# Performance work log

Measured on AMD Instinct MI355X. Metric: run time of the kernel, lower is better.

Reference implementation:

```python
import jax, jax.numpy as jnp
import numpy as np

HIDDEN = 1024
HEADS = 16
HEAD_DIM = HIDDEN // HEADS

def setup_inputs() -> dict:
    key = jax.random.key(0)
    k1, k2, k3 = jax.random.split(key, 3)
    scale = 1.0 / np.sqrt(HIDDEN)
    return {
        "x": jax.random.normal(k1, (2, 2048, HIDDEN), dtype=jnp.float32),
        "w_qkv": jax.random.normal(k2, (HIDDEN, 3 * HIDDEN), dtype=jnp.float32) * scale,
        "b_qkv": jnp.zeros((3 * HIDDEN,), dtype=jnp.float32),
        "w_out": jax.random.normal(k3, (HIDDEN, HIDDEN), dtype=jnp.float32) * scale,
        "b_out": jnp.zeros((HIDDEN,), dtype=jnp.float32),
    }

def reference(x, w_qkv, b_qkv, w_out, b_out):
    B, S, H = x.shape
    qkv = x @ w_qkv + b_qkv                              # (B,S,3H)
    qkv = qkv.reshape(B, S, 3, HEADS, HEAD_DIM)
    qkv = jnp.transpose(qkv, (2, 0, 3, 1, 4))            # (3,B,nh,S,hd)
    q, k, v = qkv[0], qkv[1], qkv[2]
    scores = jnp.einsum("bhqd,bhkd->bhqk", q, k) / np.sqrt(HEAD_DIM)
    causal = jnp.triu(jnp.ones((S, S), dtype=bool), k=1)  # True above diagonal
    scores = jnp.where(causal, -jnp.inf, scores)
    attn = jax.nn.softmax(scores, axis=-1)               # dropout: eval mode (identity)
    out = jnp.einsum("bhqk,bhkd->bhqd", attn, v)
    out = jnp.transpose(out, (0, 2, 1, 3)).reshape(B, S, H)
    return out @ w_out + b_out
```

## Files before the change

kernel.cpp:

```cpp
#include <hip/hip_runtime.h>
#include <hip/hip_bf16.h>

typedef short short8 __attribute__((ext_vector_type(8)));
typedef float f32x4 __attribute__((ext_vector_type(4)));

__device__ __forceinline__ unsigned short f2bf(float f) {
    unsigned int u = __builtin_bit_cast(unsigned int, f);
    u += 0x7fff + ((u >> 16) & 1);
    return (unsigned short)(u >> 16);
}

__global__ __launch_bounds__(256) void cast_f32_bf16(
    const float* __restrict__ in, unsigned short* __restrict__ out, int n)
{
    int i = (blockIdx.x * 256 + threadIdx.x) * 4;
    if (i >= n) return;
    float4 v = *(const float4*)(in + i);
    ushort4 o;
    o.x = f2bf(v.x); o.y = f2bf(v.y); o.z = f2bf(v.z); o.w = f2bf(v.w);
    *(ushort4*)(out + i) = o;
}

__global__ __launch_bounds__(256) void transpose_cast(
    const float* __restrict__ w, unsigned short* __restrict__ wt, int K, int N)
{
    __shared__ unsigned short tile[64 * 65];
    int k0 = blockIdx.y * 64, n0 = blockIdx.x * 64;
    for (int i = threadIdx.x; i < 64 * 64; i += 256) {
        int r = i >> 6, c = i & 63;
        tile[r * 65 + c] = f2bf(w[(size_t)(k0 + r) * N + n0 + c]);
    }
    __syncthreads();
    for (int i = threadIdx.x; i < 64 * 64; i += 256) {
        int r = i >> 6, c = i & 63;
        wt[(size_t)(n0 + r) * K + k0 + c] = tile[c * 65 + r];
    }
}

#define LDSS 40

template<bool OUT_BF16, bool QKV>
__global__ __launch_bounds__(256) void gemm_bt(
    const unsigned short* __restrict__ A,
    const unsigned short* __restrict__ Bt,
    const float* __restrict__ bias,
    void* __restrict__ C,
    unsigned short* __restrict__ vTp,
    int M, int N, int K)
{
    __shared__ __align__(16) unsigned short As[128 * LDSS];
    __shared__ __align__(16) unsigned short Bs[128 * LDSS];
    const int tid = threadIdx.x;
    const int lane = tid & 63;
    const int wave = tid >> 6;
    const int wr = wave >> 1, wc = wave & 1;
    const int m0 = blockIdx.x * 128, n0 = blockIdx.y * 128;
    const int fr = lane & 15, fq = lane >> 4;

    f32x4 acc[4][4] = {};

    const int sr = tid >> 2;
    const int sc = (tid & 3) * 8;

    for (int k0 = 0; k0 < K; k0 += 32) {
        uint4 a0 = *(const uint4*)(A  + (size_t)(m0 + sr)      * K + k0 + sc);
        uint4 a1 = *(const uint4*)(A  + (size_t)(m0 + sr + 64) * K + k0 + sc);
        uint4 b0 = *(const uint4*)(Bt + (size_t)(n0 + sr)      * K + k0 + sc);
        uint4 b1 = *(const uint4*)(Bt + (size_t)(n0 + sr + 64) * K + k0 + sc);
        __syncthreads();
        *(uint4*)(As + sr * LDSS + sc)        = a0;
        *(uint4*)(As + (sr + 64) * LDSS + sc) = a1;
        *(uint4*)(Bs + sr * LDSS + sc)        = b0;
        *(uint4*)(Bs + (sr + 64) * LDSS + sc) = b1;
        __syncthreads();

        short8 af[4], bfr[4];
#pragma unroll
        for (int i = 0; i < 4; i++)
            af[i] = *(const short8*)(As + (wr * 64 + i * 16 + fr) * LDSS + fq * 8);
#pragma unroll
        for (int j = 0; j < 4; j++)
            bfr[j] = *(const short8*)(Bs + (wc * 64 + j * 16 + fr) * LDSS + fq * 8);
#pragma unroll
        for (int i = 0; i < 4; i++)
#pragma unroll
            for (int j = 0; j < 4; j++)
                acc[i][j] = __builtin_amdgcn_mfma_f32_16x16x32_bf16(af[i], bfr[j], acc[i][j], 0, 0, 0);
    }

#pragma unroll
    for (int i = 0; i < 4; i++)
#pragma unroll
        for (int j = 0; j < 4; j++) {
            int col = n0 + wc * 64 + j * 16 + fr;
            float bv = bias[col];
            if (QKV && col >= 2048) {
                int hh = (col - 2048) >> 6, d = col & 63;
#pragma unroll
                for (int r = 0; r < 4; r++) {
                    int row = m0 + wr * 64 + i * 16 + fq * 4 + r;
                    int bb = row >> 11, s = row & 2047;
                    vTp[((size_t)(bb * 16 + hh) * 64 + d) * 2048 + s] = f2bf(acc[i][j][r] + bv);
                }
            } else {
#pragma unroll
                for (int r = 0; r < 4; r++) {
                    int row = m0 + wr * 64 + i * 16 + fq * 4 + r;
                    float v = acc[i][j][r] + bv;
                    if (OUT_BF16)
                        ((unsigned short*)C)[(size_t)row * N + col] = f2bf(v);
                    else
                        ((float*)C)[(size_t)row * N + col] = v;
                }
            }
        }
}


template<int RG0>
__device__ __forceinline__ void attn_step(
    const unsigned short* __restrict__ Ksb,
    const unsigned short* __restrict__ Vsb,
    unsigned short* __restrict__ Psw,
    const short8 (&qf)[2][2], const short8 ones,
    f32x4 (&o_acc)[2][4], f32x4 (&l_acc)[2],
    int j0, int fr, int fq,
    const int (&qrow0)[2], const bool (&diag)[2])
{
    f32x4 s[2][4];
#pragma unroll
    for (int rg = RG0; rg < 2; rg++)
#pragma unroll
        for (int t = 0; t < 4; t++)
            s[rg][t] = (f32x4){0.f, 0.f, 0.f, 0.f};

#pragma unroll
    for (int t = 0; t < 4; t++)
#pragma unroll
        for (int ks = 0; ks < 2; ks++) {
            short8 kf = *(const short8*)(Ksb + (t * 16 + fr) * 72 + ks * 32 + fq * 8);
#pragma unroll
            for (int rg = RG0; rg < 2; rg++)
                s[rg][t] = __builtin_amdgcn_mfma_f32_16x16x32_bf16(qf[rg][ks], kf, s[rg][t], 0, 0, 0);
        }

#pragma unroll
    for (int rg = RG0; rg < 2; rg++) {
#pragma unroll
        for (int t = 0; t < 4; t++)
#pragma unroll
            for (int r = 0; r < 4; r++) {
                float p = __expf(s[rg][t][r] * 0.125f - 8.0f);
                if (diag[rg]) {
                    int kcol = j0 + t * 16 + fr;
                    if (kcol > qrow0[rg] + fq * 4 + r) p = 0.f;
                }
                Psw[rg * (16 * 72) + (fq * 4 + r) * 72 + t * 16 + fr] = f2bf(p);
            }
    }

#pragma unroll
    for (int ks = 0; ks < 2; ks++) {
        short8 pf[2];
#pragma unroll
        for (int rg = RG0; rg < 2; rg++)
            pf[rg] = *(const short8*)(Psw + rg * (16 * 72) + fr * 72 + ks * 32 + fq * 8);
#pragma unroll
        for (int t = 0; t < 4; t++) {
            short8 vf = *(const short8*)(Vsb + (t * 16 + fr) * 72 + ks * 32 + fq * 8);
#pragma unroll
            for (int rg = RG0; rg < 2; rg++)
                o_acc[rg][t] = __builtin_amdgcn_mfma_f32_16x16x32_bf16(pf[rg], vf, o_acc[rg][t], 0, 0, 0);
        }
#pragma unroll
        for (int rg = RG0; rg < 2; rg++)
            l_acc[rg] = __builtin_amdgcn_mfma_f32_16x16x32_bf16(pf[rg], ones, l_acc[rg], 0, 0, 0);
    }
}

__global__ __launch_bounds__(256) void flash_attn(
    const unsigned short* __restrict__ qkv,
    const unsigned short* __restrict__ vT,
    unsigned short* __restrict__ out)
{
    const int bx = blockIdx.x, h = blockIdx.y, b = blockIdx.z;
    const int qtA = bx, qtB = 31 - bx;
    const int tid = threadIdx.x, wave = tid >> 6, lane = tid & 63;
    const int fr = lane & 15, fq = lane >> 4;
    const size_t RS = 3072;

    const unsigned short* Qb = qkv + (size_t)b * 2048 * RS + h * 64;
    const unsigned short* Kb = Qb + 1024;
    const unsigned short* Vt = vT + (size_t)(b * 16 + h) * 64 * 2048;

    __shared__ __align__(16) unsigned short Ks[2][64 * 72];
    __shared__ __align__(16) unsigned short Vs[2][64 * 72];
    __shared__ __align__(16) unsigned short Ps[4][2 * 16 * 72];

    short8 qf[2][2];
    int qrow0[2];
#pragma unroll
    for (int rg = 0; rg < 2; rg++) {
        int qt = rg ? qtB : qtA;
        qrow0[rg] = qt * 64 + wave * 16;
        const unsigned short* qrow = Qb + (size_t)(qrow0[rg] + fr) * RS;
        qf[rg][0] = *(const short8*)(qrow + fq * 8);
        qf[rg][1] = *(const short8*)(qrow + 32 + fq * 8);
    }
    short8 ones;
#pragma unroll
    for (int e = 0; e < 8; e++) ones[e] = (short)0x3F80;

    f32x4 o_acc[2][4] = {};
    f32x4 l_acc[2] = {};

    const int sr = tid >> 3;
    const int sc = (tid & 7) * 8;
    const int njt = qtB + 1;

    uint4 rk0, rk1, rv0, rv1;
    rk0 = *(const uint4*)(Kb + (size_t)sr * RS + sc);
    rk1 = *(const uint4*)(Kb + (size_t)(sr + 32) * RS + sc);
    rv0 = *(const uint4*)(Vt + (size_t)sr * 2048 + sc);
    rv1 = *(const uint4*)(Vt + (size_t)(sr + 32) * 2048 + sc);
    *(uint4*)(Ks[0] + sr * 72 + sc)        = rk0;
    *(uint4*)(Ks[0] + (sr + 32) * 72 + sc) = rk1;
    *(uint4*)(Vs[0] + sr * 72 + sc)        = rv0;
    *(uint4*)(Vs[0] + (sr + 32) * 72 + sc) = rv1;

    for (int jt = 0; jt < njt; jt++) {
        const int cur = jt & 1;
        const int j0 = jt * 64;
        const bool more = (jt + 1 < njt);
        if (more) {
            const int jn = j0 + 64;
            rk0 = *(const uint4*)(Kb + (size_t)(jn + sr) * RS + sc);
            rk1 = *(const uint4*)(Kb + (size_t)(jn + sr + 32) * RS + sc);
            rv0 = *(const uint4*)(Vt + (size_t)sr * 2048 + jn + sc);
            rv1 = *(const uint4*)(Vt + (size_t)(sr + 32) * 2048 + jn + sc);
        }
        __syncthreads();
        bool diag[2] = { jt == qtA, jt == qtB };
        if (jt <= qtA)
            attn_step<0>(Ks[cur], Vs[cur], Ps[wave], qf, ones, o_acc, l_acc, j0, fr, fq, qrow0, diag);
        else
            attn_step<1>(Ks[cur], Vs[cur], Ps[wave], qf, ones, o_acc, l_acc, j0, fr, fq, qrow0, diag);
        if (more) {
            const int nb = cur ^ 1;
            *(uint4*)(Ks[nb] + sr * 72 + sc)        = rk0;
            *(uint4*)(Ks[nb] + (sr + 32) * 72 + sc) = rk1;
            *(uint4*)(Vs[nb] + sr * 72 + sc)        = rv0;
            *(uint4*)(Vs[nb] + (sr + 32) * 72 + sc) = rv1;
        }
    }

#pragma unroll
    for (int rg = 0; rg < 2; rg++)
#pragma unroll
        for (int t = 0; t < 4; t++)
#pragma unroll
            for (int r = 0; r < 4; r++) {
                int row = qrow0[rg] + fq * 4 + r;
                out[(size_t)(b * 2048 + row) * 1024 + h * 64 + t * 16 + fr] =
                    f2bf(o_acc[rg][t][r] / l_acc[rg][r]);
            }
}

extern "C" void kernel_launch(void* const* d_in, const int* in_sizes, int n_in,
                              void* d_out, int out_size, void* d_ws, size_t ws_size,
                              hipStream_t stream) {
    const float* x      = (const float*)d_in[0];
    const float* w_qkv  = (const float*)d_in[1];
    const float* b_qkv  = (const float*)d_in[2];
    const float* w_out  = (const float*)d_in[3];
    const float* b_out  = (const float*)d_in[4];
    float* out = (float*)d_out;

    char* ws = (char*)d_ws;
    unsigned short* x_b    = (unsigned short*)(ws);
    unsigned short* wqkv_t = (unsigned short*)(ws + 8u  * 1024 * 1024);
    unsigned short* wout_t = (unsigned short*)(ws + 14u * 1024 * 1024);
    unsigned short* qkv    = (unsigned short*)(ws + 16u * 1024 * 1024);
    unsigned short* attn   = (unsigned short*)(ws + 40u * 1024 * 1024);
    unsigned short* vT     = (unsigned short*)(ws + 48u * 1024 * 1024);

    cast_f32_bf16<<<4096, 256, 0, stream>>>(x, x_b, 2 * 2048 * 1024);
    transpose_cast<<<dim3(48, 16), 256, 0, stream>>>(w_qkv, wqkv_t, 1024, 3072);
    transpose_cast<<<dim3(16, 16), 256, 0, stream>>>(w_out, wout_t, 1024, 1024);
    gemm_bt<true, true ><<<dim3(32, 24), 256, 0, stream>>>(x_b,  wqkv_t, b_qkv, qkv, vT, 4096, 3072, 1024);
    flash_attn<<<dim3(16, 16, 2), 256, 0, stream>>>(qkv, vT, attn);
    gemm_bt<false, false><<<dim3(32, 8),  256, 0, stream>>>(attn, wout_t, b_out, out, nullptr, 4096, 1024, 1024);
}
```

Baseline: 208.0 us.

## Use direct global-to-LDS async loads in GEMM and attention, pack P stores

```diff
diff --git a/kernel.cpp b/kernel.cpp
--- a/kernel.cpp
+++ b/kernel.cpp
@@ -3,11 +3,20 @@
 
 typedef short short8 __attribute__((ext_vector_type(8)));
 typedef float f32x4 __attribute__((ext_vector_type(4)));
+
+typedef const __attribute__((address_space(1))) unsigned int* gas_ptr;
+typedef __attribute__((address_space(3))) unsigned int* las_ptr;
+#define ASYNC16(g, l) __builtin_amdgcn_global_load_lds((gas_ptr)(g), (las_ptr)(l), 16, 0, 0)
 
 __device__ __forceinline__ unsigned short f2bf(float f) {
     unsigned int u = __builtin_bit_cast(unsigned int, f);
     u += 0x7fff + ((u >> 16) & 1);
     return (unsigned short)(u >> 16);
+}
+
+__device__ __forceinline__ unsigned int pkbf_trunc(float lo, float hi) {
+    return __builtin_amdgcn_perm(__builtin_bit_cast(unsigned int, hi),
+                                 __builtin_bit_cast(unsigned int, lo), 0x07060302u);
 }
 
 __global__ __launch_bounds__(256) void cast_f32_bf16(
@@ -37,10 +46,9 @@
     }
 }
 
-#define LDSS 40
 
 template<bool OUT_BF16, bool QKV>
-__global__ __launch_bounds__(256) void gemm_bt(
+__global__ __launch_bounds__(256, 3) void gemm_bt(
     const unsigned short* __restrict__ A,
     const unsigned short* __restrict__ Bt,
     const float* __restrict__ bias,
@@ -48,8 +56,8 @@
     unsigned short* __restrict__ vTp,
     int M, int N, int K)
 {
-    __shared__ __align__(16) unsigned short As[128 * LDSS];
-    __shared__ __align__(16) unsigned short Bs[128 * LDSS];
+    __shared__ __align__(16) unsigned short As[128 * 32];
+    __shared__ __align__(16) unsigned short Bs[128 * 32];
     const int tid = threadIdx.x;
     const int lane = tid & 63;
     const int wave = tid >> 6;
@@ -59,28 +67,30 @@
 
     f32x4 acc[4][4] = {};
 
-    const int sr = tid >> 2;
-    const int sc = (tid & 3) * 8;
+    const int grow = lane >> 2;
+    const int gcol = (lane & 3) * 8;
+    const unsigned short* Ag = A  + (size_t)(m0 + wave * 32 + grow) * K + gcol;
+    const unsigned short* Bg = Bt + (size_t)(n0 + wave * 32 + grow) * K + gcol;
+    unsigned short* AsW0 = As + (wave * 32) * 32;
+    unsigned short* AsW1 = As + (wave * 32 + 16) * 32;
+    unsigned short* BsW0 = Bs + (wave * 32) * 32;
+    unsigned short* BsW1 = Bs + (wave * 32 + 16) * 32;
 
     for (int k0 = 0; k0 < K; k0 += 32) {
-        uint4 a0 = *(const uint4*)(A  + (size_t)(m0 + sr)      * K + k0 + sc);
-        uint4 a1 = *(const uint4*)(A  + (size_t)(m0 + sr + 64) * K + k0 + sc);
-        uint4 b0 = *(const uint4*)(Bt + (size_t)(n0 + sr)      * K + k0 + sc);
-        uint4 b1 = *(const uint4*)(Bt + (size_t)(n0 + sr + 64) * K + k0 + sc);
         __syncthreads();
-        *(uint4*)(As + sr * LDSS + sc)        = a0;
-        *(uint4*)(As + (sr + 64) * LDSS + sc) = a1;
-        *(uint4*)(Bs + sr * LDSS + sc)        = b0;
-        *(uint4*)(Bs + (sr + 64) * LDSS + sc) = b1;
+        ASYNC16(Ag + k0,          AsW0);
+        ASYNC16(Ag + 16 * K + k0, AsW1);
+        ASYNC16(Bg + k0,          BsW0);
+        ASYNC16(Bg + 16 * K + k0, BsW1);
         __syncthreads();
 
         short8 af[4], bfr[4];
 #pragma unroll
         for (int i = 0; i < 4; i++)
-            af[i] = *(const short8*)(As + (wr * 64 + i * 16 + fr) * LDSS + fq * 8);
+            af[i] = *(const short8*)(As + (wr * 64 + i * 16 + fr) * 32 + fq * 8);
 #pragma unroll
         for (int j = 0; j < 4; j++)
-            bfr[j] = *(const short8*)(Bs + (wc * 64 + j * 16 + fr) * LDSS + fq * 8);
+            bfr[j] = *(const short8*)(Bs + (wc * 64 + j * 16 + fr) * 32 + fq * 8);
 #pragma unroll
         for (int i = 0; i < 4; i++)
 #pragma unroll
@@ -119,8 +129,8 @@
 
 template<int RG0>
 __device__ __forceinline__ void attn_step(
-    const unsigned short* __restrict__ Ksb,
-    const unsigned short* __restrict__ Vsb,
+    const unsigned short* __restrict__ Ks0, const unsigned short* __restrict__ Ks1,
+    const unsigned short* __restrict__ Vs0, const unsigned short* __restrict__ Vs1,
     unsigned short* __restrict__ Psw,
     const short8 (&qf)[2][2], const short8 ones,
     f32x4 (&o_acc)[2][4], f32x4 (&l_acc)[2],
@@ -135,39 +145,48 @@
             s[rg][t] = (f32x4){0.f, 0.f, 0.f, 0.f};
 
 #pragma unroll
-    for (int t = 0; t < 4; t++)
-#pragma unroll
-        for (int ks = 0; ks < 2; ks++) {
-            short8 kf = *(const short8*)(Ksb + (t * 16 + fr) * 72 + ks * 32 + fq * 8);
-#pragma unroll
-            for (int rg = RG0; rg < 2; rg++)
-                s[rg][t] = __builtin_amdgcn_mfma_f32_16x16x32_bf16(qf[rg][ks], kf, s[rg][t], 0, 0, 0);
+    for (int t = 0; t < 4; t++) {
+        short8 kf0 = *(const short8*)(Ks0 + (t * 16 + fr) * 32 + fq * 8);
+        short8 kf1 = *(const short8*)(Ks1 + (t * 16 + fr) * 32 + fq * 8);
+#pragma unroll
+        for (int rg = RG0; rg < 2; rg++) {
+            s[rg][t] = __builtin_amdgcn_mfma_f32_16x16x32_bf16(qf[rg][0], kf0, s[rg][t], 0, 0, 0);
+            s[rg][t] = __builtin_amdgcn_mfma_f32_16x16x32_bf16(qf[rg][1], kf1, s[rg][t], 0, 0, 0);
         }
+    }
 
 #pragma unroll
     for (int rg = RG0; rg < 2; rg++) {
-#pragma unroll
-        for (int t = 0; t < 4; t++)
+        unsigned short* prow = Psw + rg * (16 * 72);
+#pragma unroll
+        for (int t = 0; t < 4; t++) {
+            float p[4];
 #pragma unroll
             for (int r = 0; r < 4; r++) {
-                float p = __expf(s[rg][t][r] * 0.125f - 8.0f);
-                if (diag[rg]) {
-                    int kcol = j0 + t * 16 + fr;
-                    if (kcol > qrow0[rg] + fq * 4 + r) p = 0.f;
-                }
-                Psw[rg * (16 * 72) + (fq * 4 + r) * 72 + t * 16 + fr] = f2bf(p);
+                float v = __expf(s[rg][t][r] * 0.125f - 8.0f);
+                if (diag[rg] && (j0 + t * 16 + fr) > (qrow0[rg] + fq * 4 + r)) v = 0.f;
+                p[r] = v;
             }
+            unsigned int pk01 = pkbf_trunc(p[0], p[1]);
+            unsigned int pk23 = pkbf_trunc(p[2], p[3]);
+            int base = (fq * 4) * 72 + t * 16 + fr;
+            prow[base]       = (unsigned short)pk01;
+            prow[base + 72]  = (unsigned short)(pk01 >> 16);
+            prow[base + 144] = (unsigned short)pk23;
+            prow[base + 216] = (unsigned short)(pk23 >> 16);
+        }
     }
 
 #pragma unroll
     for (int ks = 0; ks < 2; ks++) {
+        const unsigned short* Vsb = ks ? Vs1 : Vs0;
         short8 pf[2];
 #pragma unroll
         for (int rg = RG0; rg < 2; rg++)
             pf[rg] = *(const short8*)(Psw + rg * (16 * 72) + fr * 72 + ks * 32 + fq * 8);
 #pragma unroll
         for (int t = 0; t < 4; t++) {
-            short8 vf = *(const short8*)(Vsb + (t * 16 + fr) * 72 + ks * 32 + fq * 8);
+            short8 vf = *(const short8*)(Vsb + (t * 16 + fr) * 32 + fq * 8);
 #pragma unroll
             for (int rg = RG0; rg < 2; rg++)
                 o_acc[rg][t] = __builtin_amdgcn_mfma_f32_16x16x32_bf16(pf[rg], vf, o_acc[rg][t], 0, 0, 0);
@@ -178,7 +197,7 @@
     }
 }
 
-__global__ __launch_bounds__(256) void flash_attn(
+__global__ __launch_bounds__(256, 4) void flash_attn(
     const unsigned short* __restrict__ qkv,
     const unsigned short* __restrict__ vT,
     unsigned short* __restrict__ out)
@@ -193,8 +212,8 @@
     const unsigned short* Kb = Qb + 1024;
     const unsigned short* Vt = vT + (size_t)(b * 16 + h) * 64 * 2048;
 
-    __shared__ __align__(16) unsigned short Ks[2][64 * 72];
-    __shared__ __align__(16) unsigned short Vs[2][64 * 72];
+    __shared__ __align__(16) unsigned short Ks[2][64 * 32];
+    __shared__ __align__(16) unsigned short Vs[2][64 * 32];
     __shared__ __align__(16) unsigned short Ps[4][2 * 16 * 72];
 
     short8 qf[2][2];
@@ -214,44 +233,32 @@
     f32x4 o_acc[2][4] = {};
     f32x4 l_acc[2] = {};
 
-    const int sr = tid >> 3;
-    const int sc = (tid & 7) * 8;
+    const int grow = lane >> 2;
+    const int gcol = (lane & 3) * 8;
+    const unsigned short* Kg = Kb + (size_t)(wave * 16 + grow) * RS + gcol;
+    const unsigned short* Vg = Vt + (size_t)(wave * 16 + grow) * 2048 + gcol;
+    unsigned short* KsW0 = Ks[0] + (wave * 16) * 32;
+    unsigned short* KsW1 = Ks[1] + (wave * 16) * 32;
+    unsigned short* VsW0 = Vs[0] + (wave * 16) * 32;
+    unsigned short* VsW1 = Vs[1] + (wave * 16) * 32;
+
     const int njt = qtB + 1;
-
-    uint4 rk0, rk1, rv0, rv1;
-    rk0 = *(const uint4*)(Kb + (size_t)sr * RS + sc);
-    rk1 = *(const uint4*)(Kb + (size_t)(sr + 32) * RS + sc);
-    rv0 = *(const uint4*)(Vt + (size_t)sr * 2048 + sc);
-    rv1 = *(const uint4*)(Vt + (size_t)(sr + 32) * 2048 + sc);
-    *(uint4*)(Ks[0] + sr * 72 + sc)        = rk0;
-    *(uint4*)(Ks[0] + (sr + 32) * 72 + sc) = rk1;
-    *(uint4*)(Vs[0] + sr * 72 + sc)        = rv0;
-    *(uint4*)(Vs[0] + (sr + 32) * 72 + sc) = rv1;
-
     for (int jt = 0; jt < njt; jt++) {
-        const int cur = jt & 1;
         const int j0 = jt * 64;
-        const bool more = (jt + 1 < njt);
-        if (more) {
-            const int jn = j0 + 64;
-            rk0 = *(const uint4*)(Kb + (size_t)(jn + sr) * RS + sc);
-            rk1 = *(const uint4*)(Kb + (size_t)(jn + sr + 32) * RS + sc);
-            rv0 = *(const uint4*)(Vt + (size_t)sr * 2048 + jn + sc);
-            rv1 = *(const uint4*)(Vt + (size_t)(sr + 32) * 2048 + jn + sc);
-        }
         __syncthreads();
+        ASYNC16(Kg + (size_t)j0 * RS,      KsW0);
+        ASYNC16(Kg + (size_t)j0 * RS + 32, KsW1);
+        ASYNC16(Vg + j0,      VsW0);
+        ASYNC16(Vg + j0 + 32, VsW1);
+        __syncthreads();
+
         bool diag[2] = { jt == qtA, jt == qtB };
         if (jt <= qtA)
-            attn_step<0>(Ks[cur], Vs[cur], Ps[wave], qf, ones, o_acc, l_acc, j0, fr, fq, qrow0, diag);
+            attn_step<0>(Ks[0], Ks[1], Vs[0], Vs[1], Ps[wave], qf, ones,
+                         o_acc, l_acc, j0, fr, fq, qrow0, diag);
         else
-            attn_step<1>(Ks[cur], Vs[cur], Ps[wave], qf, ones, o_acc, l_acc, j0, fr, fq, qrow0, diag);
-        if (more) {
-            const int nb = cur ^ 1;
-            *(uint4*)(Ks[nb] + sr * 72 + sc)        = rk0;
-            *(uint4*)(Ks[nb] + (sr + 32) * 72 + sc) = rk1;
-            *(uint4*)(Vs[nb] + sr * 72 + sc)        = rv0;
-            *(uint4*)(Vs[nb] + (sr + 32) * 72 + sc) = rv1;
-        }
+            attn_step<1>(Ks[0], Ks[1], Vs[0], Vs[1], Ps[wave], qf, ones,
+                         o_acc, l_acc, j0, fr, fq, qrow0, diag);
     }
 
 #pragma unroll
```

Result: faster. 202.1 us (-2.9%).
